# Optimization experiments

Hardware: AMD Instinct MI355X
Metric: run time of the kernel (lower is better)

Reference implementation:

```python
import jax, jax.numpy as jnp
import numpy as np

N_IDX = 3_276_800   # total indices shared across all bags
N_BAGS = 16_384     # number of bags (offsets length)
NUM_EMB = 2_000_000 # vocabulary rows per table
DIM = 3             # embedding dim fixed by the module


def setup_inputs() -> dict:
    key = jax.random.key(0)
    k1, k2, k3, k4, k5 = jax.random.split(key, 5)
    eb_input = jax.random.randint(k1, (N_IDX,), 0, NUM_EMB, dtype=jnp.int32)
    eb_offset = jnp.sort(jax.random.randint(k2, (N_BAGS,), 0, N_IDX, dtype=jnp.int32))
    eb_offset = eb_offset.at[0].set(0)  # EmbeddingBag requires offsets[0] == 0
    W0 = jax.random.normal(k3, (NUM_EMB, DIM), dtype=jnp.float32)
    W1 = jax.random.normal(k4, (NUM_EMB, DIM), dtype=jnp.float32)
    W2 = jax.random.normal(k5, (NUM_EMB, DIM), dtype=jnp.float32)
    return {"eb_input": eb_input, "eb_offset": eb_offset, "W0": W0, "W1": W1, "W2": W2}


def _embedding_bag_sum(W, idx, seg_ids, num_bags):
    # gather rows then segment-sum within each bag -> [num_bags, DIM]
    return jax.ops.segment_sum(W[idx], seg_ids, num_segments=num_bags)


def reference(eb_input, eb_offset, W0, W1, W2):
    num_bags = eb_offset.shape[0]
    # bag id of each index position, from the offsets (shared by all 21 bags)
    seg_ids = jnp.searchsorted(eb_offset, jnp.arange(eb_input.shape[0], dtype=eb_offset.dtype), side="right") - 1
    rows = []
    # each group reuses ONE table k times ([module]*k aliases the same module),
    # so cat(k copies of [B,3]).sum(0) == k * per_bag.sum(0)
    for W, mult in ((W0, 5.0), (W1, 10.0), (W2, 6.0)):
        per_bag = _embedding_bag_sum(W, eb_input, seg_ids, num_bags)  # [B, 3]
        rows.append(mult * per_bag.sum(axis=0))                      # [3]
    return jnp.stack(rows)  # [3, 3]
```

## Files before the change

### kernel.cpp

```cpp
#include <hip/hip_runtime.h>


constexpr int BLOCK = 256;
constexpr int WAVES = BLOCK / 64;

constexpr int CBITS = 14;
constexpr int CROWS = 1 << CBITS;
constexpr int MAXKC = 128;
constexpr int GP    = 512;
constexpr int CAPC  = 112;
constexpr int HB    = 1024;
constexpr int SUMG  = 1920;


__global__ __launch_bounds__(BLOCK) void partition_kernel(
    const int* __restrict__ idx,
    unsigned short* __restrict__ region,
    int* __restrict__ counts_T,
    int n, int K)
{
    __shared__ __align__(16) unsigned short buf[MAXKC][CAPC];
    __shared__ int rcnt[MAXKC];

    for (int b = threadIdx.x; b < K; b += BLOCK) rcnt[b] = 0;
    __syncthreads();

    const int g = blockIdx.x;
    const int4* idx4 = (const int4*)idx;
    const int n4 = n >> 2;
    const int per = (n4 + GP - 1) / GP;
    const int start = g * per;
    const int end = min(start + per, n4);

    int i = start + threadIdx.x;
    bool have = i < end;
    int4 cur;
    if (have) cur = idx4[i];
    while (have) {
        const int inext = i + BLOCK;
        const bool hnext = inext < end;
        int4 nxt;
        if (hnext) nxt = idx4[inext];
        {
            int b0 = cur.x >> CBITS, l0 = cur.x & (CROWS - 1);
            int p0 = atomicAdd(&rcnt[b0], 1);
            if (p0 < CAPC) buf[b0][p0] = (unsigned short)l0;
            int b1 = cur.y >> CBITS, l1 = cur.y & (CROWS - 1);
            int p1 = atomicAdd(&rcnt[b1], 1);
            if (p1 < CAPC) buf[b1][p1] = (unsigned short)l1;
            int b2 = cur.z >> CBITS, l2 = cur.z & (CROWS - 1);
            int p2 = atomicAdd(&rcnt[b2], 1);
            if (p2 < CAPC) buf[b2][p2] = (unsigned short)l2;
            int b3 = cur.w >> CBITS, l3 = cur.w & (CROWS - 1);
            int p3 = atomicAdd(&rcnt[b3], 1);
            if (p3 < CAPC) buf[b3][p3] = (unsigned short)l3;
        }
        i = inext; have = hnext; cur = nxt;
    }
    if (g == 0 && threadIdx.x == 0) {
        for (int t = n4 << 2; t < n; ++t) {
            int x = idx[t];
            int b = x >> CBITS, lo = x & (CROWS - 1);
            int pos = atomicAdd(&rcnt[b], 1);
            if (pos < CAPC) buf[b][pos] = (unsigned short)lo;
        }
    }
    __syncthreads();

    for (int b = threadIdx.x; b < K; b += BLOCK) {
        int c = rcnt[b]; if (c > CAPC) c = CAPC;
        unsigned short* cell = region + ((size_t)b * GP + g) * CAPC;
        const int ng = (c + 7) >> 3;
        for (int j = 0; j < ng; ++j)
            *(uint4*)(cell + j * 8) = *(const uint4*)&buf[b][j * 8];
        counts_T[b * GP + g] = c;
    }
}


__global__ __launch_bounds__(HB) void hist_build_kernel(
    const unsigned short* __restrict__ region,
    const int* __restrict__ counts_T,
    int* __restrict__ counts)
{
    __shared__ unsigned int histp[CROWS / 2];
    __shared__ int scnt[GP];
    const int b = blockIdx.x;

    for (int j = threadIdx.x; j < CROWS / 2; j += HB) histp[j] = 0u;
    for (int g = threadIdx.x; g < GP; g += HB) scnt[g] = counts_T[b * GP + g];
    __syncthreads();

    constexpr int GPC = CAPC / 8;
    constexpr int NG  = GP * GPC;
    const uint4* reg4 = (const uint4*)(region + (size_t)b * GP * CAPC);
    for (int j = threadIdx.x; j < NG; j += HB) {
        int g = j / GPC;
        int q = j - g * GPC;
        uint4 v = reg4[j];
        int valid = scnt[g] - q * 8;
        if (valid >= 8) {
            atomicAdd(&histp[(v.x & 0xFFFFu) >> 1], 1u << (((v.x) & 1u) << 4));
            atomicAdd(&histp[(v.x >> 16) >> 1],     1u << (((v.x >> 16) & 1u) << 4));
            atomicAdd(&histp[(v.y & 0xFFFFu) >> 1], 1u << (((v.y) & 1u) << 4));
            atomicAdd(&histp[(v.y >> 16) >> 1],     1u << (((v.y >> 16) & 1u) << 4));
            atomicAdd(&histp[(v.z & 0xFFFFu) >> 1], 1u << (((v.z) & 1u) << 4));
            atomicAdd(&histp[(v.z >> 16) >> 1],     1u << (((v.z >> 16) & 1u) << 4));
            atomicAdd(&histp[(v.w & 0xFFFFu) >> 1], 1u << (((v.w) & 1u) << 4));
            atomicAdd(&histp[(v.w >> 16) >> 1],     1u << (((v.w >> 16) & 1u) << 4));
        } else if (valid > 0) {
            unsigned vv[4] = {v.x, v.y, v.z, v.w};
#pragma unroll
            for (int h = 0; h < 4; ++h) {
                unsigned lo0 = vv[h] & 0xFFFFu, lo1 = vv[h] >> 16;
                if (valid > 2 * h)     atomicAdd(&histp[lo0 >> 1], 1u << ((lo0 & 1u) << 4));
                if (valid > 2 * h + 1) atomicAdd(&histp[lo1 >> 1], 1u << ((lo1 & 1u) << 4));
            }
        }
    }
    __syncthreads();

    int4* out4 = (int4*)(counts + ((size_t)b << CBITS));
    for (int j = threadIdx.x; j < CROWS / 4; j += HB) {
        unsigned u0 = histp[2 * j], u1 = histp[2 * j + 1];
        int4 val;
        val.x = (int)(u0 & 0xFFFFu);
        val.y = (int)(u0 >> 16);
        val.z = (int)(u1 & 0xFFFFu);
        val.w = (int)(u1 >> 16);
        out4[j] = val;
    }
}


__global__ __launch_bounds__(BLOCK) void weighted_sum_v4(
    const int* __restrict__ counts,
    const float* __restrict__ W0,
    const float* __restrict__ W1,
    const float* __restrict__ W2,
    float* __restrict__ partials,
    int nrows)
{
    float s[9];
#pragma unroll
    for (int k = 0; k < 9; ++k) s[k] = 0.0f;
    const int tid = blockIdx.x * BLOCK + threadIdx.x;
    const int stride = gridDim.x * BLOCK;
    const int nt = nrows >> 2;
    const int4*   c4  = (const int4*)counts;
    const float4* W04 = (const float4*)W0;
    const float4* W14 = (const float4*)W1;
    const float4* W24 = (const float4*)W2;
    for (int t = tid; t < nt; t += stride) {
        int4 ci = c4[t];
        float c0 = (float)ci.x, c1 = (float)ci.y, c2 = (float)ci.z, c3 = (float)ci.w;
        {
            float4 A = W04[3*t], B = W04[3*t+1], C = W04[3*t+2];
            s[0] += c0*A.x + c1*A.w + c2*B.z + c3*C.y;
            s[1] += c0*A.y + c1*B.x + c2*B.w + c3*C.z;
            s[2] += c0*A.z + c1*B.y + c2*C.x + c3*C.w;
        }
        {
            float4 A = W14[3*t], B = W14[3*t+1], C = W14[3*t+2];
            s[3] += c0*A.x + c1*A.w + c2*B.z + c3*C.y;
            s[4] += c0*A.y + c1*B.x + c2*B.w + c3*C.z;
            s[5] += c0*A.z + c1*B.y + c2*C.x + c3*C.w;
        }
        {
            float4 A = W24[3*t], B = W24[3*t+1], C = W24[3*t+2];
            s[6] += c0*A.x + c1*A.w + c2*B.z + c3*C.y;
            s[7] += c0*A.y + c1*B.x + c2*B.w + c3*C.z;
            s[8] += c0*A.z + c1*B.y + c2*C.x + c3*C.w;
        }
    }
    if (tid == 0) {
        for (int r = nt << 2; r < nrows; ++r) {
            float c = (float)counts[r];
            int o = r * 3;
            s[0] += c * W0[o]; s[1] += c * W0[o+1]; s[2] += c * W0[o+2];
            s[3] += c * W1[o]; s[4] += c * W1[o+1]; s[5] += c * W1[o+2];
            s[6] += c * W2[o]; s[7] += c * W2[o+1]; s[8] += c * W2[o+2];
        }
    }
#pragma unroll
    for (int k = 0; k < 9; ++k) {
#pragma unroll
        for (int off = 32; off > 0; off >>= 1)
            s[k] += __shfl_down(s[k], off, 64);
    }
    __shared__ float lds[WAVES][9];
    const int lane = threadIdx.x & 63;
    const int wave = threadIdx.x >> 6;
    if (lane == 0) {
#pragma unroll
        for (int k = 0; k < 9; ++k) lds[wave][k] = s[k];
    }
    __syncthreads();
    if (threadIdx.x < 9) {
        float acc = 0.0f;
#pragma unroll
        for (int w = 0; w < WAVES; ++w) acc += lds[w][threadIdx.x];
        partials[blockIdx.x * 9 + threadIdx.x] = acc;
    }
}


__global__ __launch_bounds__(BLOCK) void eb_final(
    const float* __restrict__ partials, int nblocks, float* __restrict__ out)
{
    float s[9];
#pragma unroll
    for (int k = 0; k < 9; ++k) s[k] = 0.0f;
    for (int i = threadIdx.x; i < nblocks; i += BLOCK) {
#pragma unroll
        for (int k = 0; k < 9; ++k) s[k] += partials[i * 9 + k];
    }
#pragma unroll
    for (int k = 0; k < 9; ++k) {
#pragma unroll
        for (int off = 32; off > 0; off >>= 1)
            s[k] += __shfl_down(s[k], off, 64);
    }
    __shared__ float lds[WAVES][9];
    const int lane = threadIdx.x & 63;
    const int wave = threadIdx.x >> 6;
    if (lane == 0) {
#pragma unroll
        for (int k = 0; k < 9; ++k) lds[wave][k] = s[k];
    }
    __syncthreads();
    if (threadIdx.x == 0) {
        float tot[9];
#pragma unroll
        for (int k = 0; k < 9; ++k) {
            float acc = 0.0f;
#pragma unroll
            for (int w = 0; w < WAVES; ++w) acc += lds[w][k];
            tot[k] = acc;
        }
        const float mult[3] = {5.0f, 10.0f, 6.0f};
#pragma unroll
        for (int r = 0; r < 3; ++r)
#pragma unroll
            for (int c = 0; c < 3; ++c)
                out[r * 3 + c] = mult[r] * tot[r * 3 + c];
    }
}


__global__ __launch_bounds__(BLOCK) void zero_counts(int* __restrict__ counts, int n) {
    int4* c4 = (int4*)counts;
    const int n4 = n >> 2;
    const int tid = blockIdx.x * BLOCK + threadIdx.x;
    const int stride = gridDim.x * BLOCK;
    int4 z = {0, 0, 0, 0};
    for (int i = tid; i < n4; i += stride) c4[i] = z;
    if (tid == 0)
        for (int i = n4 << 2; i < n; ++i) counts[i] = 0;
}

__global__ __launch_bounds__(BLOCK) void hist_kernel(
    const int* __restrict__ idx, int* __restrict__ counts, int n) {
    const int4* idx4 = (const int4*)idx;
    const int n4 = n >> 2;
    const int tid = blockIdx.x * BLOCK + threadIdx.x;
    const int stride = gridDim.x * BLOCK;
    for (int i = tid; i < n4; i += stride) {
        int4 v = idx4[i];
        atomicAdd(&counts[v.x], 1);
        atomicAdd(&counts[v.y], 1);
        atomicAdd(&counts[v.z], 1);
        atomicAdd(&counts[v.w], 1);
    }
    if (tid == 0)
        for (int i = n4 << 2; i < n; ++i) atomicAdd(&counts[idx[i]], 1);
}

extern "C" void kernel_launch(void* const* d_in, const int* in_sizes, int n_in,
                              void* d_out, int out_size, void* d_ws, size_t ws_size,
                              hipStream_t stream) {
    const int*   idx = (const int*)d_in[0];
    const float* W0  = (const float*)d_in[2];
    const float* W1  = (const float*)d_in[3];
    const float* W2  = (const float*)d_in[4];
    float* out = (float*)d_out;

    const int n     = in_sizes[0];
    const int nrows = in_sizes[2] / 3;
    const int K     = (nrows + CROWS - 1) >> CBITS;

    const size_t region_bytes  = (size_t)K * GP * CAPC * sizeof(unsigned short);
    const size_t countsT_bytes = (size_t)K * GP * sizeof(int);
    const size_t counts_bytes  = (size_t)K * CROWS * sizeof(int);
    const size_t partS_bytes   = (size_t)SUMG * 9 * sizeof(float);

    const size_t need_part = region_bytes + countsT_bytes + counts_bytes + partS_bytes;
    const size_t need_hist = (size_t)nrows * sizeof(int) + partS_bytes;

    if (K <= MAXKC && ws_size >= need_part) {
        unsigned short* region   = (unsigned short*)d_ws;
        int*   counts_T = (int*)  ((char*)d_ws + region_bytes);
        int*   counts   = (int*)  ((char*)d_ws + region_bytes + countsT_bytes);
        float* partials = (float*)((char*)d_ws + region_bytes + countsT_bytes + counts_bytes);

        partition_kernel<<<GP, BLOCK, 0, stream>>>(idx, region, counts_T, n, K);
        hist_build_kernel<<<K, HB, 0, stream>>>(region, counts_T, counts);
        weighted_sum_v4<<<SUMG, BLOCK, 0, stream>>>(counts, W0, W1, W2, partials, nrows);
        eb_final<<<1, BLOCK, 0, stream>>>(partials, SUMG, out);
    } else if (ws_size >= need_hist) {
        int*   counts   = (int*)d_ws;
        float* partials = (float*)((char*)d_ws + (size_t)nrows * sizeof(int));
        zero_counts<<<512, BLOCK, 0, stream>>>(counts, nrows);
        hist_kernel<<<1280, BLOCK, 0, stream>>>(idx, counts, n);
        weighted_sum_v4<<<SUMG, BLOCK, 0, stream>>>(counts, W0, W1, W2, partials, nrows);
        eb_final<<<1, BLOCK, 0, stream>>>(partials, SUMG, out);
    }
}
```

Before: 138.6 us.

## Fuse histogram build with weighted sum and drop final reduction kernel

The histogram-build kernel now goes straight on to the weighted sum over its own slice of rows, reading counts from LDS. This removes the global counts array round trip and the separate weighted-sum and final-reduce kernels; each block adds its scaled partial into the output with atomics, and the partition kernel zeroes the output first. The bucket size is halved (CBITS 13, CAP 64), which doubles the block count to about 245 blocks of 1024 threads. The risk is lower memory-level parallelism for the 72MB weight stream with far fewer threads than the old 1920-block sum, plus float atomics making the summation order nondeterministic.

```diff
diff --git a/kernel.cpp b/kernel.cpp
--- a/kernel.cpp
+++ b/kernel.cpp
@@ -2,26 +2,29 @@
 
 
 constexpr int BLOCK = 256;
+constexpr int FB    = 1024;
 constexpr int WAVES = BLOCK / 64;
-
-constexpr int CBITS = 14;
+constexpr int FWAVES = FB / 64;
+
+constexpr int CBITS = 13;
 constexpr int CROWS = 1 << CBITS;
-constexpr int MAXKC = 128;
+constexpr int MAXK  = 256;
 constexpr int GP    = 512;
-constexpr int CAPC  = 112;
-constexpr int HB    = 1024;
-constexpr int SUMG  = 1920;
+constexpr int CAP   = 64;
+constexpr int GPC   = CAP / 8;
 
 
 __global__ __launch_bounds__(BLOCK) void partition_kernel(
     const int* __restrict__ idx,
     unsigned short* __restrict__ region,
     int* __restrict__ counts_T,
+    float* __restrict__ out,
     int n, int K)
 {
-    __shared__ __align__(16) unsigned short buf[MAXKC][CAPC];
-    __shared__ int rcnt[MAXKC];
-
+    __shared__ __align__(16) unsigned short buf[MAXK][CAP];
+    __shared__ int rcnt[MAXK];
+
+    if (blockIdx.x == 0 && threadIdx.x < 9) out[threadIdx.x] = 0.0f;
     for (int b = threadIdx.x; b < K; b += BLOCK) rcnt[b] = 0;
     __syncthreads();
 
@@ -44,16 +47,16 @@
         {
             int b0 = cur.x >> CBITS, l0 = cur.x & (CROWS - 1);
             int p0 = atomicAdd(&rcnt[b0], 1);
-            if (p0 < CAPC) buf[b0][p0] = (unsigned short)l0;
+            if (p0 < CAP) buf[b0][p0] = (unsigned short)l0;
             int b1 = cur.y >> CBITS, l1 = cur.y & (CROWS - 1);
             int p1 = atomicAdd(&rcnt[b1], 1);
-            if (p1 < CAPC) buf[b1][p1] = (unsigned short)l1;
+            if (p1 < CAP) buf[b1][p1] = (unsigned short)l1;
             int b2 = cur.z >> CBITS, l2 = cur.z & (CROWS - 1);
             int p2 = atomicAdd(&rcnt[b2], 1);
-            if (p2 < CAPC) buf[b2][p2] = (unsigned short)l2;
+            if (p2 < CAP) buf[b2][p2] = (unsigned short)l2;
             int b3 = cur.w >> CBITS, l3 = cur.w & (CROWS - 1);
             int p3 = atomicAdd(&rcnt[b3], 1);
-            if (p3 < CAPC) buf[b3][p3] = (unsigned short)l3;
+            if (p3 < CAP) buf[b3][p3] = (unsigned short)l3;
         }
         i = inext; have = hnext; cur = nxt;
     }
@@ -62,14 +65,14 @@
             int x = idx[t];
             int b = x >> CBITS, lo = x & (CROWS - 1);
             int pos = atomicAdd(&rcnt[b], 1);
-            if (pos < CAPC) buf[b][pos] = (unsigned short)lo;
+            if (pos < CAP) buf[b][pos] = (unsigned short)lo;
         }
     }
     __syncthreads();
 
     for (int b = threadIdx.x; b < K; b += BLOCK) {
-        int c = rcnt[b]; if (c > CAPC) c = CAPC;
-        unsigned short* cell = region + ((size_t)b * GP + g) * CAPC;
+        int c = rcnt[b]; if (c > CAP) c = CAP;
+        unsigned short* cell = region + ((size_t)b * GP + g) * CAP;
         const int ng = (c + 7) >> 3;
         for (int j = 0; j < ng; ++j)
             *(uint4*)(cell + j * 8) = *(const uint4*)&buf[b][j * 8];
@@ -78,25 +81,30 @@
 }
 
 
-__global__ __launch_bounds__(HB) void hist_build_kernel(
+__global__ __launch_bounds__(FB) void fused_hist_sum(
     const unsigned short* __restrict__ region,
     const int* __restrict__ counts_T,
-    int* __restrict__ counts)
+    const float* __restrict__ W0,
+    const float* __restrict__ W1,
+    const float* __restrict__ W2,
+    float* __restrict__ out,
+    int nrows)
 {
     __shared__ unsigned int histp[CROWS / 2];
     __shared__ int scnt[GP];
+    __shared__ float lred[FWAVES][9];
     const int b = blockIdx.x;
-
-    for (int j = threadIdx.x; j < CROWS / 2; j += HB) histp[j] = 0u;
-    for (int g = threadIdx.x; g < GP; g += HB) scnt[g] = counts_T[b * GP + g];
-    __syncthreads();
-
-    constexpr int GPC = CAPC / 8;
-    constexpr int NG  = GP * GPC;
-    const uint4* reg4 = (const uint4*)(region + (size_t)b * GP * CAPC);
-    for (int j = threadIdx.x; j < NG; j += HB) {
-        int g = j / GPC;
-        int q = j - g * GPC;
+    const int tid = threadIdx.x;
+
+    for (int j = tid; j < CROWS / 2; j += FB) histp[j] = 0u;
+    for (int g = tid; g < GP; g += FB) scnt[g] = counts_T[b * GP + g];
+    __syncthreads();
+
+    constexpr int NG = GP * GPC;
+    const uint4* reg4 = (const uint4*)(region + (size_t)b * GP * CAP);
+    for (int j = tid; j < NG; j += FB) {
+        int g = j >> 3;
+        int q = j & 7;
         uint4 v = reg4[j];
         int valid = scnt[g] - q * 8;
         if (valid >= 8) {
@@ -120,40 +128,21 @@
     }
     __syncthreads();
 
-    int4* out4 = (int4*)(counts + ((size_t)b << CBITS));
-    for (int j = threadIdx.x; j < CROWS / 4; j += HB) {
-        unsigned u0 = histp[2 * j], u1 = histp[2 * j + 1];
-        int4 val;
-        val.x = (int)(u0 & 0xFFFFu);
-        val.y = (int)(u0 >> 16);
-        val.z = (int)(u1 & 0xFFFFu);
-        val.w = (int)(u1 >> 16);
-        out4[j] = val;
-    }
-}
-
-
-__global__ __launch_bounds__(BLOCK) void weighted_sum_v4(
-    const int* __restrict__ counts,
-    const float* __restrict__ W0,
-    const float* __restrict__ W1,
-    const float* __restrict__ W2,
-    float* __restrict__ partials,
-    int nrows)
-{
     float s[9];
 #pragma unroll
     for (int k = 0; k < 9; ++k) s[k] = 0.0f;
-    const int tid = blockIdx.x * BLOCK + threadIdx.x;
-    const int stride = gridDim.x * BLOCK;
-    const int nt = nrows >> 2;
-    const int4*   c4  = (const int4*)counts;
-    const float4* W04 = (const float4*)W0;
-    const float4* W14 = (const float4*)W1;
-    const float4* W24 = (const float4*)W2;
-    for (int t = tid; t < nt; t += stride) {
-        int4 ci = c4[t];
-        float c0 = (float)ci.x, c1 = (float)ci.y, c2 = (float)ci.z, c3 = (float)ci.w;
+
+    const int rbase = b << CBITS;
+    int nr = nrows - rbase; if (nr > CROWS) nr = CROWS;
+    const int ntg = nr >> 2;
+    const float4* W04 = (const float4*)(W0 + (size_t)rbase * 3);
+    const float4* W14 = (const float4*)(W1 + (size_t)rbase * 3);
+    const float4* W24 = (const float4*)(W2 + (size_t)rbase * 3);
+
+    for (int t = tid; t < ntg; t += FB) {
+        unsigned u0 = histp[2 * t], u1 = histp[2 * t + 1];
+        float c0 = (float)(u0 & 0xFFFFu), c1 = (float)(u0 >> 16);
+        float c2 = (float)(u1 & 0xFFFFu), c3 = (float)(u1 >> 16);
         {
             float4 A = W04[3*t], B = W04[3*t+1], C = W04[3*t+2];
             s[0] += c0*A.x + c1*A.w + c2*B.z + c3*C.y;
@@ -174,81 +163,42 @@
         }
     }
     if (tid == 0) {
-        for (int r = nt << 2; r < nrows; ++r) {
-            float c = (float)counts[r];
-            int o = r * 3;
+        for (int lr = ntg << 2; lr < nr; ++lr) {
+            unsigned w = histp[lr >> 1];
+            float c = (float)((lr & 1) ? (w >> 16) : (w & 0xFFFFu));
+            int o = (rbase + lr) * 3;
             s[0] += c * W0[o]; s[1] += c * W0[o+1]; s[2] += c * W0[o+2];
             s[3] += c * W1[o]; s[4] += c * W1[o+1]; s[5] += c * W1[o+2];
             s[6] += c * W2[o]; s[7] += c * W2[o+1]; s[8] += c * W2[o+2];
         }
     }
+
 #pragma unroll
     for (int k = 0; k < 9; ++k) {
 #pragma unroll
         for (int off = 32; off > 0; off >>= 1)
             s[k] += __shfl_down(s[k], off, 64);
     }
-    __shared__ float lds[WAVES][9];
-    const int lane = threadIdx.x & 63;
-    const int wave = threadIdx.x >> 6;
+    const int lane = tid & 63;
+    const int wave = tid >> 6;
     if (lane == 0) {
 #pragma unroll
-        for (int k = 0; k < 9; ++k) lds[wave][k] = s[k];
-    }
-    __syncthreads();
-    if (threadIdx.x < 9) {
+        for (int k = 0; k < 9; ++k) lred[wave][k] = s[k];
+    }
+    __syncthreads();
+    if (tid < 9) {
         float acc = 0.0f;
 #pragma unroll
-        for (int w = 0; w < WAVES; ++w) acc += lds[w][threadIdx.x];
-        partials[blockIdx.x * 9 + threadIdx.x] = acc;
-    }
-}
-
-
-__global__ __launch_bounds__(BLOCK) void eb_final(
-    const float* __restrict__ partials, int nblocks, float* __restrict__ out)
-{
-    float s[9];
-#pragma unroll
-    for (int k = 0; k < 9; ++k) s[k] = 0.0f;
-    for (int i = threadIdx.x; i < nblocks; i += BLOCK) {
-#pragma unroll
-        for (int k = 0; k < 9; ++k) s[k] += partials[i * 9 + k];
-    }
-#pragma unroll
-    for (int k = 0; k < 9; ++k) {
-#pragma unroll
-        for (int off = 32; off > 0; off >>= 1)
-            s[k] += __shfl_down(s[k], off, 64);
-    }
-    __shared__ float lds[WAVES][9];
-    const int lane = threadIdx.x & 63;
-    const int wave = threadIdx.x >> 6;
-    if (lane == 0) {
-#pragma unroll
-        for (int k = 0; k < 9; ++k) lds[wave][k] = s[k];
-    }
-    __syncthreads();
-    if (threadIdx.x == 0) {
-        float tot[9];
-#pragma unroll
-        for (int k = 0; k < 9; ++k) {
-            float acc = 0.0f;
-#pragma unroll
-            for (int w = 0; w < WAVES; ++w) acc += lds[w][k];
-            tot[k] = acc;
-        }
-        const float mult[3] = {5.0f, 10.0f, 6.0f};
-#pragma unroll
-        for (int r = 0; r < 3; ++r)
-#pragma unroll
-            for (int c = 0; c < 3; ++c)
-                out[r * 3 + c] = mult[r] * tot[r * 3 + c];
-    }
-}
-
-
-__global__ __launch_bounds__(BLOCK) void zero_counts(int* __restrict__ counts, int n) {
+        for (int w = 0; w < FWAVES; ++w) acc += lred[w][tid];
+        const float mult9[9] = {5.0f,5.0f,5.0f, 10.0f,10.0f,10.0f, 6.0f,6.0f,6.0f};
+        atomicAdd(&out[tid], mult9[tid] * acc);
+    }
+}
+
+
+__global__ __launch_bounds__(BLOCK) void zero_counts(int* __restrict__ counts, int n,
+                                                     float* __restrict__ out) {
+    if (blockIdx.x == 0 && threadIdx.x < 9) out[threadIdx.x] = 0.0f;
     int4* c4 = (int4*)counts;
     const int n4 = n >> 2;
     const int tid = blockIdx.x * BLOCK + threadIdx.x;
@@ -276,6 +226,78 @@
         for (int i = n4 << 2; i < n; ++i) atomicAdd(&counts[idx[i]], 1);
 }
 
+__global__ __launch_bounds__(BLOCK) void weighted_sum_atomic(
+    const int* __restrict__ counts,
+    const float* __restrict__ W0,
+    const float* __restrict__ W1,
+    const float* __restrict__ W2,
+    float* __restrict__ out,
+    int nrows)
+{
+    float s[9];
+#pragma unroll
+    for (int k = 0; k < 9; ++k) s[k] = 0.0f;
+    const int tid = blockIdx.x * BLOCK + threadIdx.x;
+    const int stride = gridDim.x * BLOCK;
+    const int nt = nrows >> 2;
+    const int4*   c4  = (const int4*)counts;
+    const float4* W04 = (const float4*)W0;
+    const float4* W14 = (const float4*)W1;
+    const float4* W24 = (const float4*)W2;
+    for (int t = tid; t < nt; t += stride) {
+        int4 ci = c4[t];
+        float c0 = (float)ci.x, c1 = (float)ci.y, c2 = (float)ci.z, c3 = (float)ci.w;
+        {
+            float4 A = W04[3*t], B = W04[3*t+1], C = W04[3*t+2];
+            s[0] += c0*A.x + c1*A.w + c2*B.z + c3*C.y;
+            s[1] += c0*A.y + c1*B.x + c2*B.w + c3*C.z;
+            s[2] += c0*A.z + c1*B.y + c2*C.x + c3*C.w;
+        }
+        {
+            float4 A = W14[3*t], B = W14[3*t+1], C = W14[3*t+2];
+            s[3] += c0*A.x + c1*A.w + c2*B.z + c3*C.y;
+            s[4] += c0*A.y + c1*B.x + c2*B.w + c3*C.z;
+            s[5] += c0*A.z + c1*B.y + c2*C.x + c3*C.w;
+        }
+        {
+            float4 A = W24[3*t], B = W24[3*t+1], C = W24[3*t+2];
+            s[6] += c0*A.x + c1*A.w + c2*B.z + c3*C.y;
+            s[7] += c0*A.y + c1*B.x + c2*B.w + c3*C.z;
+            s[8] += c0*A.z + c1*B.y + c2*C.x + c3*C.w;
+        }
+    }
+    if (tid == 0) {
+        for (int r = nt << 2; r < nrows; ++r) {
+            float c = (float)counts[r];
+            int o = r * 3;
+            s[0] += c * W0[o]; s[1] += c * W0[o+1]; s[2] += c * W0[o+2];
+            s[3] += c * W1[o]; s[4] += c * W1[o+1]; s[5] += c * W1[o+2];
+            s[6] += c * W2[o]; s[7] += c * W2[o+1]; s[8] += c * W2[o+2];
+        }
+    }
+#pragma unroll
+    for (int k = 0; k < 9; ++k) {
+#pragma unroll
+        for (int off = 32; off > 0; off >>= 1)
+            s[k] += __shfl_down(s[k], off, 64);
+    }
+    __shared__ float lds[WAVES][9];
+    const int lane = threadIdx.x & 63;
+    const int wave = threadIdx.x >> 6;
+    if (lane == 0) {
+#pragma unroll
+        for (int k = 0; k < 9; ++k) lds[wave][k] = s[k];
+    }
+    __syncthreads();
+    if (threadIdx.x < 9) {
+        float acc = 0.0f;
+#pragma unroll
+        for (int w = 0; w < WAVES; ++w) acc += lds[w][threadIdx.x];
+        const float mult9[9] = {5.0f,5.0f,5.0f, 10.0f,10.0f,10.0f, 6.0f,6.0f,6.0f};
+        atomicAdd(&out[threadIdx.x], mult9[threadIdx.x] * acc);
+    }
+}
+
 extern "C" void kernel_launch(void* const* d_in, const int* in_sizes, int n_in,
                               void* d_out, int out_size, void* d_ws, size_t ws_size,
                               hipStream_t stream) {
@@ -289,30 +311,22 @@
     const int nrows = in_sizes[2] / 3;
     const int K     = (nrows + CROWS - 1) >> CBITS;
 
-    const size_t region_bytes  = (size_t)K * GP * CAPC * sizeof(unsigned short);
+    const size_t region_bytes  = (size_t)K * GP * CAP * sizeof(unsigned short);
     const size_t countsT_bytes = (size_t)K * GP * sizeof(int);
-    const size_t counts_bytes  = (size_t)K * CROWS * sizeof(int);
-    const size_t partS_bytes   = (size_t)SUMG * 9 * sizeof(float);
-
-    const size_t need_part = region_bytes + countsT_bytes + counts_bytes + partS_bytes;
-    const size_t need_hist = (size_t)nrows * sizeof(int) + partS_bytes;
-
-    if (K <= MAXKC && ws_size >= need_part) {
+
+    const size_t need_part = region_bytes + countsT_bytes;
+    const size_t need_hist = (size_t)nrows * sizeof(int);
+
+    if (K <= MAXK && ws_size >= need_part) {
         unsigned short* region   = (unsigned short*)d_ws;
-        int*   counts_T = (int*)  ((char*)d_ws + region_bytes);
-        int*   counts   = (int*)  ((char*)d_ws + region_bytes + countsT_bytes);
-        float* partials = (float*)((char*)d_ws + region_bytes + countsT_bytes + counts_bytes);
-
-        partition_kernel<<<GP, BLOCK, 0, stream>>>(idx, region, counts_T, n, K);
-        hist_build_kernel<<<K, HB, 0, stream>>>(region, counts_T, counts);
-        weighted_sum_v4<<<SUMG, BLOCK, 0, stream>>>(counts, W0, W1, W2, partials, nrows);
-        eb_final<<<1, BLOCK, 0, stream>>>(partials, SUMG, out);
+        int* counts_T = (int*)((char*)d_ws + region_bytes);
+
+        partition_kernel<<<GP, BLOCK, 0, stream>>>(idx, region, counts_T, out, n, K);
+        fused_hist_sum<<<K, FB, 0, stream>>>(region, counts_T, W0, W1, W2, out, nrows);
     } else if (ws_size >= need_hist) {
-        int*   counts   = (int*)d_ws;
-        float* partials = (float*)((char*)d_ws + (size_t)nrows * sizeof(int));
-        zero_counts<<<512, BLOCK, 0, stream>>>(counts, nrows);
+        int* counts = (int*)d_ws;
+        zero_counts<<<512, BLOCK, 0, stream>>>(counts, n == 0 ? nrows : nrows, out);
         hist_kernel<<<1280, BLOCK, 0, stream>>>(idx, counts, n);
-        weighted_sum_v4<<<SUMG, BLOCK, 0, stream>>>(counts, W0, W1, W2, partials, nrows);
-        eb_final<<<1, BLOCK, 0, stream>>>(partials, SUMG, out);
-    }
-}
+        weighted_sum_atomic<<<1920, BLOCK, 0, stream>>>(counts, W0, W1, W2, out, nrows);
+    }
+}
```

Result: faster. 128.7 us (-7.2%).
